# Kernel optimization log

Hardware: AMD Instinct MI355X
Metric: run time of the kernel (lower is better)

## Reference

```python
import jax, jax.numpy as jnp
import numpy as np

Q_UPPER = 64  # number of quantization bins for upper-layer distributions
CLIP_LO, CLIP_HI = 1e-15, 1e15


def setup_inputs() -> dict:
    key = jax.random.key(0)
    k = jax.random.split(key, 6)
    B, NU, NL, QU, QL = 256, 64, 64, Q_UPPER, 64
    w_init = 0.1
    P = jax.random.uniform(k[0], (B, NL, QL), dtype=jnp.float32)
    weight = jax.random.uniform(k[1], (NU, NL), minval=-w_init, maxval=w_init, dtype=jnp.float32)
    bias_abs = jax.random.uniform(k[2], (NU, 1), minval=-w_init, maxval=w_init, dtype=jnp.float32)
    bias_q = jax.random.uniform(k[3], (NU, 1), minval=-w_init, maxval=w_init, dtype=jnp.float32)
    lambda_abs = jax.random.uniform(k[4], (NU, 1), minval=0.0, maxval=1.0, dtype=jnp.float32)
    lambda_q = jax.random.uniform(k[5], (NU, 1), minval=0.0, maxval=1.0, dtype=jnp.float32)
    return {"P": P, "weight": weight, "bias_abs": bias_abs, "bias_q": bias_q,
            "lambda_abs": lambda_abs, "lambda_q": lambda_q}


def reference(P, weight, bias_abs, bias_q, lambda_abs, lambda_q):
    # P: [B, n_lower, q_lower]; weight: [n_upper, n_lower]; biases/lambdas: [n_upper, 1]
    QU = Q_UPPER
    QL = P.shape[2]
    s1 = jnp.arange(QU, dtype=P.dtype) / QU          # upper bin centers
    s0 = jnp.arange(QL, dtype=P.dtype) / QL          # lower bin centers
    diff2 = (s0[None, :] - s1[:, None]) ** 2          # [QU, QL]
    # D = exp(-diff2); T = D**weight = exp(-weight * diff2), permuted to [NU, NL, QU, QL]
    T = jnp.exp(-weight[:, :, None, None] * diff2[None, None, :, :])
    # batched GEMV over q_lower: Pw[i,j,k,l] = sum_m T[j,k,l,m] * P[i,k,m]
    Pw = jnp.einsum('jklm,ikm->ijkl', T, P)           # [B, NU, NL, QU]
    logPw = jnp.log(jnp.clip(Pw, CLIP_LO, CLIP_HI))
    logsum = jnp.sum(logPw, axis=2)                   # [B, NU, QU]
    sq = jnp.arange(QU, dtype=P.dtype)[None, :] / QU  # [1, QU]
    exponent_B = (-bias_q * (sq - lambda_q) ** 2
                  - bias_abs * jnp.abs(sq - lambda_abs))  # [NU, QU]
    logsumB = logsum + exponent_B[None, :, :]
    return jax.nn.softmax(logsumB, axis=2)            # [B, NU, QU]
```

## Files before the change

kernel.cpp:

```cpp
#include <hip/hip_runtime.h>
#include <hip/hip_fp16.h>


#define NUP 64
#define NLOW 64
#define QUP 64
#define QLOW 64

__global__ __launch_bounds__(512, 8)
void drn_kernel(const float* __restrict__ P,
                const float* __restrict__ weight,
                const float* __restrict__ bias_abs,
                const float* __restrict__ bias_q,
                const float* __restrict__ lambda_abs,
                const float* __restrict__ lambda_q,
                float* __restrict__ out)
{
    __shared__ float2 lds_n[NLOW * QUP];

    const int i    = blockIdx.x >> 2;
    const int jq   = blockIdx.x & 3;
    const int tid  = threadIdx.x;
    const int lane = tid & 63;
    const int wv   = __builtin_amdgcn_readfirstlane(tid >> 6);

    float t0 = 0.f, t1 = 0.f, t2 = 0.f, t3 = 0.f, t4 = 0.f, t5 = 0.f, t6 = 0.f;
    {
        const int kk = lane >> 3;
        const int mc = lane & 7;
        const int k  = wv * 8 + kk;
        const float* Pr = P + ((size_t)i * NLOW + k) * QLOW + mc * 8;
        const float4 pa = *reinterpret_cast<const float4*>(Pr);
        const float4 pb = *reinterpret_cast<const float4*>(Pr + 4);

        const float s0 = (float)(mc * 8) * 0.015625f;
#define ACCM(PV, S) { float f = (PV); const float s_ = (S); \
        t0 += f; f *= s_; t1 += f; f *= s_; t2 += f; f *= s_; t3 += f; \
        f *= s_; t4 += f; f *= s_; t5 += f; f *= s_; t6 += f; }
        ACCM(pa.x, s0);
        ACCM(pa.y, s0 + 0.015625f);
        ACCM(pa.z, s0 + 0.03125f);
        ACCM(pa.w, s0 + 0.046875f);
        ACCM(pb.x, s0 + 0.0625f);
        ACCM(pb.y, s0 + 0.078125f);
        ACCM(pb.z, s0 + 0.09375f);
        ACCM(pb.w, s0 + 0.109375f);
#undef ACCM
#define RED7(OFF) { t0 += __shfl_xor(t0, OFF, 64); t1 += __shfl_xor(t1, OFF, 64); \
        t2 += __shfl_xor(t2, OFF, 64); t3 += __shfl_xor(t3, OFF, 64); \
        t4 += __shfl_xor(t4, OFF, 64); t5 += __shfl_xor(t5, OFF, 64); \
        t6 += __shfl_xor(t6, OFF, 64); }
        RED7(1) RED7(2) RED7(4)
#undef RED7
    }

    const float s1l = (float)lane * 0.015625f;
    {
        const float A2 = 0.50039123f;
        const float C6 = 1.0f / 6.0f;
        const float z  = -s1l;
        const float z2 = z * z, z3 = z2 * z, z4 = z2 * z2, z5 = z4 * z, z6 = z4 * z2;
        const float b10 = z2,        b11 = 2.f * z;
        const float b20 = z4,        b21 = 4.f * z3, b22 = 6.f * z2, b23 = 4.f * z;
        const float b30 = z6,        b31 = 6.f * z5, b32 = 15.f * z4,
                    b33 = 20.f * z3, b34 = 15.f * z2, b35 = 6.f * z;

#pragma unroll
        for (int kk = 0; kk < 8; ++kk) {
            const int k = wv * 8 + kk;
            const float m0 = __shfl(t0, kk * 8, 64);
            const float m1 = __shfl(t1, kk * 8, 64);
            const float m2 = __shfl(t2, kk * 8, 64);
            const float m3 = __shfl(t3, kk * 8, 64);
            const float m4 = __shfl(t4, kk * 8, 64);
            const float m5 = __shfl(t5, kk * 8, 64);
            const float m6 = __shfl(t6, kk * 8, 64);

            const float inv = 1.0f / m0;
            const float M1 = fmaf(b10, m0, fmaf(b11, m1, m2));
            const float M2 = fmaf(b20, m0, fmaf(b21, m1, fmaf(b22, m2,
                             fmaf(b23, m3, m4))));
            const float M3 = fmaf(b30, m0, fmaf(b31, m1, fmaf(b32, m2,
                             fmaf(b33, m3, fmaf(b34, m4, fmaf(b35, m5, m6))))));

            const float n1 = M1 * inv;
            const float n2 = A2 * M2 * inv;
            const float n3 = C6 * M3 * inv;

            union { __half2 h; float f; } pk;
            pk.h = __floats2half2_rn(n2, n3);
            float2 e; e.x = n1; e.y = pk.f;
            lds_n[k * QUP + lane] = e;
        }
    }
    __syncthreads();

    const float* __restrict__ w0r = weight + (size_t)(jq * 16 + wv * 2 + 0) * NLOW;
    const float* __restrict__ w1r = weight + (size_t)(jq * 16 + wv * 2 + 1) * NLOW;

    float pr0 = 1.f, pr1 = 1.f;
    for (int k8 = 0; k8 < 8; ++k8) {
        float w0[8], w1[8];
#pragma unroll
        for (int kk = 0; kk < 8; ++kk) {
            w0[kk] = w0r[k8 * 8 + kk];
            w1[kk] = w1r[k8 * 8 + kk];
        }
#pragma unroll
        for (int kk = 0; kk < 8; ++kk) {
            const float2 v = lds_n[(k8 * 8 + kk) * QUP + lane];
            union { float f; __half2 h; } pk; pk.f = v.y;
            const float2 n23 = __half22float2(pk.h);
#define STEPJ(W, PR) { const float w_ = (W); \
            float t = fmaf(-w_, n23.y, n23.x); \
            t = fmaf(-w_, t, v.x); \
            PR *= fmaf(-w_, t, 1.0f); }
            STEPJ(w0[kk], pr0)
            STEPJ(w1[kk], pr1)
#undef STEPJ
        }
    }

    const float LOG2E = 1.4426950408889634f;
    auto finish = [&](float prv, int jj) {
        const int j = jq * 16 + wv * 2 + jj;
        const float dq = s1l - lambda_q[j];
        float y = __log2f(prv);
        y = fmaf(-bias_q[j] * LOG2E, dq * dq, y);
        y = fmaf(-bias_abs[j] * LOG2E, fabsf(s1l - lambda_abs[j]), y);
        const float e = exp2f(y);
        float s = e;
#pragma unroll
        for (int off = 32; off >= 1; off >>= 1)
            s += __shfl_xor(s, off, 64);
        out[((size_t)i * NUP + j) * QUP + lane] = e / s;
    };
    finish(pr0, 0);
    finish(pr1, 1);
}

extern "C" void kernel_launch(void* const* d_in, const int* in_sizes, int n_in,
                              void* d_out, int out_size, void* d_ws, size_t ws_size,
                              hipStream_t stream) {
    const float* P          = (const float*)d_in[0];
    const float* weight     = (const float*)d_in[1];
    const float* bias_abs   = (const float*)d_in[2];
    const float* bias_q     = (const float*)d_in[3];
    const float* lambda_abs = (const float*)d_in[4];
    const float* lambda_q   = (const float*)d_in[5];
    (void)in_sizes; (void)n_in; (void)out_size; (void)d_ws; (void)ws_size;

    drn_kernel<<<dim3(1024), dim3(512), 0, stream>>>(
        P, weight, bias_abs, bias_q, lambda_abs, lambda_q, (float*)d_out);
}
```

Baseline: 79.47 us.

## Split moment precompute into a separate kernel writing a global workspace plane

The per-batch moment and normalisation precompute moves into its own kernel, which runs once per batch element and writes the packed n1/n2/n3 plane to the workspace in global memory. A second kernel with smaller 256-thread blocks and twice as many blocks reads that plane straight from global memory to form the per-upper-neuron products. This removes the old fourfold redundant recomputation of the moments in every block, along with the LDS staging and the barrier. The cost is an extra kernel launch, an 8 MB workspace write, and eight global re-reads of each batch's plane, which may not stay in L2.

```diff
diff --git a/kernel.cpp b/kernel.cpp
--- a/kernel.cpp
+++ b/kernel.cpp
@@ -7,19 +7,10 @@
 #define QUP 64
 #define QLOW 64
 
-__global__ __launch_bounds__(512, 8)
-void drn_kernel(const float* __restrict__ P,
-                const float* __restrict__ weight,
-                const float* __restrict__ bias_abs,
-                const float* __restrict__ bias_q,
-                const float* __restrict__ lambda_abs,
-                const float* __restrict__ lambda_q,
-                float* __restrict__ out)
+__global__ __launch_bounds__(512, 2)
+void drn_prep(const float* __restrict__ P, float2* __restrict__ nplane)
 {
-    __shared__ float2 lds_n[NLOW * QUP];
-
-    const int i    = blockIdx.x >> 2;
-    const int jq   = blockIdx.x & 3;
+    const int i    = blockIdx.x;
     const int tid  = threadIdx.x;
     const int lane = tid & 63;
     const int wv   = __builtin_amdgcn_readfirstlane(tid >> 6);
@@ -90,16 +81,37 @@
             union { __half2 h; float f; } pk;
             pk.h = __floats2half2_rn(n2, n3);
             float2 e; e.x = n1; e.y = pk.f;
-            lds_n[k * QUP + lane] = e;
+            nplane[((size_t)i * NLOW + k) * QUP + lane] = e;
         }
     }
-    __syncthreads();
+}
 
-    const float* __restrict__ w0r = weight + (size_t)(jq * 16 + wv * 2 + 0) * NLOW;
-    const float* __restrict__ w1r = weight + (size_t)(jq * 16 + wv * 2 + 1) * NLOW;
+__global__ __launch_bounds__(256, 8)
+void drn_main(const float2* __restrict__ nplane,
+              const float* __restrict__ weight,
+              const float* __restrict__ bias_abs,
+              const float* __restrict__ bias_q,
+              const float* __restrict__ lambda_abs,
+              const float* __restrict__ lambda_q,
+              float* __restrict__ out)
+{
+    const int i    = blockIdx.x & 255;
+    const int jq   = blockIdx.x >> 8;
+    const int tid  = threadIdx.x;
+    const int lane = tid & 63;
+    const int wv   = __builtin_amdgcn_readfirstlane(tid >> 6);
+    const int j0   = jq * 8 + wv * 2;
+
+    const float* __restrict__ w0r = weight + (size_t)(j0 + 0) * NLOW;
+    const float* __restrict__ w1r = weight + (size_t)(j0 + 1) * NLOW;
+    const float2* __restrict__ nb = nplane + (size_t)i * (NLOW * QUP) + lane;
 
     float pr0 = 1.f, pr1 = 1.f;
     for (int k8 = 0; k8 < 8; ++k8) {
+        float2 v[8];
+#pragma unroll
+        for (int kk = 0; kk < 8; ++kk)
+            v[kk] = nb[(size_t)(k8 * 8 + kk) * QUP];
         float w0[8], w1[8];
 #pragma unroll
         for (int kk = 0; kk < 8; ++kk) {
@@ -108,12 +120,11 @@
         }
 #pragma unroll
         for (int kk = 0; kk < 8; ++kk) {
-            const float2 v = lds_n[(k8 * 8 + kk) * QUP + lane];
-            union { float f; __half2 h; } pk; pk.f = v.y;
+            union { float f; __half2 h; } pk; pk.f = v[kk].y;
             const float2 n23 = __half22float2(pk.h);
 #define STEPJ(W, PR) { const float w_ = (W); \
             float t = fmaf(-w_, n23.y, n23.x); \
-            t = fmaf(-w_, t, v.x); \
+            t = fmaf(-w_, t, v[kk].x); \
             PR *= fmaf(-w_, t, 1.0f); }
             STEPJ(w0[kk], pr0)
             STEPJ(w1[kk], pr1)
@@ -121,9 +132,10 @@
         }
     }
 
+    const float s1l   = (float)lane * 0.015625f;
     const float LOG2E = 1.4426950408889634f;
     auto finish = [&](float prv, int jj) {
-        const int j = jq * 16 + wv * 2 + jj;
+        const int j = j0 + jj;
         const float dq = s1l - lambda_q[j];
         float y = __log2f(prv);
         y = fmaf(-bias_q[j] * LOG2E, dq * dq, y);
@@ -148,8 +160,11 @@
     const float* bias_q     = (const float*)d_in[3];
     const float* lambda_abs = (const float*)d_in[4];
     const float* lambda_q   = (const float*)d_in[5];
-    (void)in_sizes; (void)n_in; (void)out_size; (void)d_ws; (void)ws_size;
+    (void)in_sizes; (void)n_in; (void)out_size; (void)ws_size;
 
-    drn_kernel<<<dim3(1024), dim3(512), 0, stream>>>(
-        P, weight, bias_abs, bias_q, lambda_abs, lambda_q, (float*)d_out);
+    float2* nplane = (float2*)d_ws;
+
+    drn_prep<<<dim3(256), dim3(512), 0, stream>>>(P, nplane);
+    drn_main<<<dim3(2048), dim3(256), 0, stream>>>(
+        nplane, weight, bias_abs, bias_q, lambda_abs, lambda_q, (float*)d_out);
 }
```

Result: slower. 85.33 us (+7.4%).
